# Optimization experiments

Measured on AMD Instinct MI355X. Metric: run time of the kernel, lower is better.

## Reference

```python
import jax, jax.numpy as jnp
import numpy as np

B, T, C, H, N, FFN = 4, 1024, 2048, 32, 64, 7168
HEAD_DIVISOR = 8.0
EPS = 1e-5


def setup_inputs() -> dict:
    key = jax.random.key(0)
    ks = jax.random.split(key, 30)
    rn = lambda k, s, sc=0.02: jax.random.normal(k, s, jnp.float32) * sc
    ru = lambda k, s: jax.random.uniform(k, s, jnp.float32)
    return {
        "x": jax.random.normal(ks[0], (B, T, C), jnp.float32),
        "att_shift": jax.random.normal(ks[1], (B, C), jnp.float32),
        "wkv_state": jax.random.normal(ks[2], (B, H, N, N), jnp.float32) * 0.1,
        "ffn_shift": jax.random.normal(ks[3], (B, C), jnp.float32),
        "ln1_w": jnp.ones((C,), jnp.float32), "ln1_b": jnp.zeros((C,), jnp.float32),
        "ln2_w": jnp.ones((C,), jnp.float32), "ln2_b": jnp.zeros((C,), jnp.float32),
        "mix_k": ru(ks[4], (C,)), "mix_v": ru(ks[5], (C,)),
        "mix_r": ru(ks[6], (C,)), "mix_g": ru(ks[7], (C,)),
        "Wr": rn(ks[8], (C, C)), "Wk": rn(ks[9], (C, C)), "Wv": rn(ks[10], (C, C)),
        "Wg": rn(ks[11], (C, C)), "Wo": rn(ks[12], (C, C)),
        "time_decay": jax.random.normal(ks[13], (H, N), jnp.float32) * 0.5,
        "time_faaaa": jax.random.normal(ks[14], (H, N), jnp.float32) * 0.1,
        "gn_w": jnp.ones((C,), jnp.float32), "gn_b": jnp.zeros((C,), jnp.float32),
        "cmix_k": ru(ks[15], (C,)), "cmix_r": ru(ks[16], (C,)),
        "Wck": rn(ks[17], (C, FFN)), "Wcr": rn(ks[18], (C, C)), "Wcv": rn(ks[19], (FFN, C)),
    }


def _ln(z, w, b):
    m = z.mean(-1, keepdims=True)
    v = z.var(-1, keepdims=True)
    return (z - m) / jnp.sqrt(v + EPS) * w + b


def _shift(x, shift_state):
    # prepend carried last-token state, drop final position
    return jnp.concatenate([shift_state[:, None, :], x[:, :-1]], axis=1)


def reference(x, att_shift, wkv_state, ffn_shift, ln1_w, ln1_b, ln2_w, ln2_b,
              mix_k, mix_v, mix_r, mix_g, Wr, Wk, Wv, Wg, Wo,
              time_decay, time_faaaa, gn_w, gn_b, cmix_k, cmix_r, Wck, Wcr, Wcv):
    Bb, Tt, Cc = x.shape

    # ---- TimeMix ----
    x1 = _ln(x, ln1_w, ln1_b)
    xx = _shift(x1, att_shift)
    xk = x1 * mix_k + xx * (1 - mix_k)
    xv = x1 * mix_v + xx * (1 - mix_v)
    xr = x1 * mix_r + xx * (1 - mix_r)
    xg = x1 * mix_g + xx * (1 - mix_g)
    r = (xr @ Wr).reshape(Bb, Tt, H, N)
    k = (xk @ Wk).reshape(Bb, Tt, H, N)
    v = (xv @ Wv).reshape(Bb, Tt, H, N)
    g = jax.nn.silu(xg @ Wg)

    w = jnp.exp(-jnp.exp(time_decay))[None, :, :, None]  # [1,H,N,1] decay on k-index
    u = time_faaaa[None, :, :, None]                      # [1,H,N,1] bonus on current token

    def step(S, rkv):  # S: [B,H,N,N] (k-index i, v-index j)
        rr, kk, vv = rkv
        kv = kk[..., :, None] * vv[..., None, :]          # [B,H,N,N]
        y = jnp.einsum('bhi,bhij->bhj', rr, S + u * kv)
        return S * w + kv, y

    rkv = (jnp.moveaxis(r, 1, 0), jnp.moveaxis(k, 1, 0), jnp.moveaxis(v, 1, 0))
    new_wkv, ys = jax.lax.scan(step, wkv_state, rkv)      # ys: [T,B,H,N]
    att = jnp.moveaxis(ys, 0, 1)                          # [B,T,H,N]

    # GroupNorm(n_head groups) on att / head_size_divisor
    z = att / HEAD_DIVISOR
    m = z.mean(-1, keepdims=True)
    var = z.var(-1, keepdims=True)
    z = (z - m) / jnp.sqrt(var + EPS)
    z = z * gn_w.reshape(H, N) + gn_b.reshape(H, N)
    att_out = (z.reshape(Bb, Tt, Cc) * g) @ Wo

    x = x + att_out

    # ---- ChannelMix ----
    x2 = _ln(x, ln2_w, ln2_b)
    xx2 = _shift(x2, ffn_shift)
    xck = x2 * cmix_k + xx2 * (1 - cmix_k)
    xcr = x2 * cmix_r + xx2 * (1 - cmix_r)
    kk = jnp.square(jax.nn.relu(xck @ Wck))
    kv = kk @ Wcv
    ffn_out = jax.nn.sigmoid(xcr @ Wcr) * kv
    x = x + ffn_out

    return x, x1[:, -1], new_wkv, x2[:, -1]
```

## Files before the change

kernel.cpp:

```cpp
#include <hip/hip_runtime.h>
#include <cstdint>
#include <cstddef>

typedef unsigned short u16;
typedef unsigned int u32;
typedef short bf16x8 __attribute__((ext_vector_type(8)));
typedef unsigned short u16x4 __attribute__((ext_vector_type(4)));
typedef unsigned short u16x8 __attribute__((ext_vector_type(8)));
typedef float f32x4 __attribute__((ext_vector_type(4)));

#define DEV __device__ __forceinline__

constexpr int Bb = 4, Tt = 1024, Cc = 2048, Hh = 32, Nd = 64, FF = 7168;
constexpr int BT = Bb * Tt;
constexpr int NCH = 16;

DEV u16 f2bf(float f) {
  union { float f; unsigned u; } un; un.f = f;
  unsigned r = un.u + 0x7FFFu + ((un.u >> 16) & 1u);
  return (u16)(r >> 16);
}
DEV float bf2f(u16 h) {
  union { unsigned u; float f; } un; un.u = ((unsigned)h) << 16;
  return un.f;
}
DEV void gll16(const u16* gp, u16* lp) {
  __builtin_amdgcn_global_load_lds(
      (const __attribute__((address_space(1))) unsigned int*)gp,
      (__attribute__((address_space(3))) unsigned int*)lp,
      16, 0, 0);
}

DEV void transp_body(const float* __restrict__ W, u16* __restrict__ Wt,
                     int Kk, int Nn, float (*tile)[33]) {
  int n0 = blockIdx.x * 32, k0 = blockIdx.y * 32;
  int tx = threadIdx.x & 31, ty = threadIdx.x >> 5;
  #pragma unroll
  for (int r = 0; r < 32; r += 8)
    tile[r + ty][tx] = W[(size_t)(k0 + r + ty) * Nn + n0 + tx];
  __syncthreads();
  #pragma unroll
  for (int r = 0; r < 32; r += 8)
    Wt[(size_t)(n0 + r + ty) * Kk + k0 + tx] = f2bf(tile[tx][r + ty]);
}

__global__ void transpose_to_bf16(const float* __restrict__ W, u16* __restrict__ Wt,
                                  int Kk, int Nn) {
  __shared__ float tile[32][33];
  transp_body(W, Wt, Kk, Nn, tile);
}

__global__ void transpose6_cc(const float* __restrict__ W0, const float* __restrict__ W1,
                              const float* __restrict__ W2, const float* __restrict__ W3,
                              const float* __restrict__ W4, const float* __restrict__ W5,
                              u16* __restrict__ T0, u16* __restrict__ T1,
                              u16* __restrict__ T2, u16* __restrict__ T3,
                              u16* __restrict__ T4, u16* __restrict__ T5) {
  __shared__ float tile[32][33];
  const int z = blockIdx.z;
  const float* W = (z == 0) ? W0 : (z == 1) ? W1 : (z == 2) ? W2 :
                   (z == 3) ? W3 : (z == 4) ? W4 : W5;
  u16* T = (z == 0) ? T0 : (z == 1) ? T1 : (z == 2) ? T2 :
           (z == 3) ? T3 : (z == 4) ? T4 : T5;
  transp_body(W, T, Cc, Cc, tile);
}

DEV void block_ln(const float* __restrict__ src, int tid, float* red,
                  float vals[8], float& mean, float& inv) {
  float s = 0.f, ss = 0.f;
  #pragma unroll
  for (int i = 0; i < 8; i++) {
    float t = src[tid + i * 256];
    vals[i] = t; s += t; ss += t * t;
  }
  #pragma unroll
  for (int m = 1; m < 64; m <<= 1) { s += __shfl_xor(s, m); ss += __shfl_xor(ss, m); }
  int lane = tid & 63, wv = tid >> 6;
  __syncthreads();
  if (lane == 0) { red[wv] = s; red[4 + wv] = ss; }
  __syncthreads();
  s = red[0] + red[1] + red[2] + red[3];
  ss = red[4] + red[5] + red[6] + red[7];
  mean = s * (1.f / Cc);
  float var = ss * (1.f / Cc) - mean * mean;
  inv = rsqrtf(var + 1e-5f);
}

__global__ __launch_bounds__(256)
void ln_mix4(const float* __restrict__ x, const float* __restrict__ shift,
             const float* __restrict__ w, const float* __restrict__ b,
             const float* __restrict__ mk, const float* __restrict__ mv,
             const float* __restrict__ mr, const float* __restrict__ mg,
             u16* __restrict__ xk, u16* __restrict__ xv,
             u16* __restrict__ xr, u16* __restrict__ xg,
             float* __restrict__ last) {
  int row = blockIdx.x;
  int t = row & (Tt - 1), bb = row >> 10;
  int tid = threadIdx.x;
  __shared__ float red[8];
  const float* cur = x + (size_t)row * Cc;
  float cv[8], pv[8], cm, ci, pm = 0.f, pi = 1.f;
  block_ln(cur, tid, red, cv, cm, ci);
  bool t0 = (t == 0);
  const float* prev = t0 ? (shift + (size_t)bb * Cc) : (cur - Cc);
  if (!t0) {
    block_ln(prev, tid, red, pv, pm, pi);
  } else {
    #pragma unroll
    for (int i = 0; i < 8; i++) pv[i] = prev[tid + i * 256];
  }
  size_t o = (size_t)row * Cc;
  bool isLast = (t == Tt - 1);
  #pragma unroll
  for (int i = 0; i < 8; i++) {
    int c = tid + i * 256;
    float xc = (cv[i] - cm) * ci * w[c] + b[c];
    float xp = t0 ? pv[i] : (pv[i] - pm) * pi * w[c] + b[c];
    xk[o + c] = f2bf(xp + mk[c] * (xc - xp));
    xv[o + c] = f2bf(xp + mv[c] * (xc - xp));
    xr[o + c] = f2bf(xp + mr[c] * (xc - xp));
    xg[o + c] = f2bf(xp + mg[c] * (xc - xp));
    if (isLast) last[(size_t)bb * Cc + c] = xc;
  }
}

__global__ __launch_bounds__(256)
void ln_mix2(const float* __restrict__ x, const float* __restrict__ shift,
             const float* __restrict__ w, const float* __restrict__ b,
             const float* __restrict__ ck, const float* __restrict__ cr,
             u16* __restrict__ xck, u16* __restrict__ xcr,
             float* __restrict__ last) {
  int row = blockIdx.x;
  int t = row & (Tt - 1), bb = row >> 10;
  int tid = threadIdx.x;
  __shared__ float red[8];
  const float* cur = x + (size_t)row * Cc;
  float cv[8], pv[8], cm, ci, pm = 0.f, pi = 1.f;
  block_ln(cur, tid, red, cv, cm, ci);
  bool t0 = (t == 0);
  const float* prev = t0 ? (shift + (size_t)bb * Cc) : (cur - Cc);
  if (!t0) {
    block_ln(prev, tid, red, pv, pm, pi);
  } else {
    #pragma unroll
    for (int i = 0; i < 8; i++) pv[i] = prev[tid + i * 256];
  }
  size_t o = (size_t)row * Cc;
  bool isLast = (t == Tt - 1);
  #pragma unroll
  for (int i = 0; i < 8; i++) {
    int c = tid + i * 256;
    float xc = (cv[i] - cm) * ci * w[c] + b[c];
    float xp = t0 ? pv[i] : (pv[i] - pm) * pi * w[c] + b[c];
    xck[o + c] = f2bf(xp + ck[c] * (xc - xp));
    xcr[o + c] = f2bf(xp + cr[c] * (xc - xp));
    if (isLast) last[(size_t)bb * Cc + c] = xc;
  }
}


DEV int swzoff(int row, int off) {
  return (row << 7) +
         (off ^ ((((row >> 1) & 1) << 4) | (((row >> 2) & 1) << 5) | (((row >> 3) & 1) << 6)));
}

DEV void stage_half(const u16* __restrict__ gbase, int ldK, u16* slot, int tid) {
  #pragma unroll
  for (int c2 = 0; c2 < 2; c2++) {
    const int D = c2 * 8192 + tid * 16;
    const int row = D >> 7;
    const int off = (D & 127) ^ ((((row >> 1) & 1) << 4) | (((row >> 2) & 1) << 5) | (((row >> 3) & 1) << 6));
    gll16(gbase + (size_t)row * ldK + (off >> 1), (u16*)((char*)slot + D));
  }
}

template <int EPI, int NB>
DEV void g256_core(const u16* __restrict__ A, const u16* __restrict__ Bt,
                   int N, int K,
                   float* __restrict__ Co, u16* __restrict__ Cb,
                   const float* __restrict__ X1, const float* __restrict__ X2,
                   u16 (*lds)[8192], int m0, int n0, int act) {
  const int tid = threadIdx.x;
  const int w = tid >> 6, lane = tid & 63;
  const int l15 = lane & 15, l4 = lane >> 4;
  const int wm = (w & 3) * 64;
  const int wn = (w >> 2) * (NB * 64);
  const int ahalf = wm >> 7;
  const int arow0 = wm & 127;
  const int bhalf = (NB == 2) ? (w >> 2) : 0;
  const int nt = K >> 6;

  const u16* Ag = A + (size_t)m0 * K;
  const u16* Bg = Bt + (size_t)n0 * K;

  f32x4 acc[4][NB * 4] = {};
  bf16x8 a[4][2];

  stage_half(Ag, K, lds[0], tid);
  stage_half(Ag + (size_t)128 * K, K, lds[1], tid);
  stage_half(Bg, K, lds[4], tid);
  if constexpr (NB == 2) stage_half(Bg + (size_t)128 * K, K, lds[5], tid);
  if (nt > 1) {
    stage_half(Ag + 64, K, lds[2], tid);
    stage_half(Ag + (size_t)128 * K + 64, K, lds[3], tid);
    asm volatile("s_waitcnt vmcnt(4)" ::: "memory");
  } else {
    asm volatile("s_waitcnt vmcnt(0)" ::: "memory");
  }
  asm volatile("s_barrier" ::: "memory");

  for (int t = 0; t < nt; t++) {
    const int buf = t & 1;
    const char* Aslot = (const char*)lds[buf * 2 + ahalf];
    const char* Bslot = (const char*)lds[4 + buf * NB + bhalf];

#define G256_PHASE(p)                                                                       \
    {                                                                                       \
      constexpr int nh = (p) >> 1, kh = (p) & 1;                                            \
      if constexpr ((p) < 2) {                                                              \
        _Pragma("unroll")                                                                   \
        for (int mf = 0; mf < 4; mf++) {                                                    \
          const int row = arow0 + mf * 16 + l15;                                            \
          a[mf][kh] = *(const bf16x8*)(Aslot + swzoff(row, kh * 64 + l4 * 16));             \
        }                                                                                   \
      }                                                                                     \
      bf16x8 bfr[2 * NB];                                                                   \
      _Pragma("unroll")                                                                     \
      for (int j = 0; j < 2 * NB; j++) {                                                    \
        const int row = (NB == 2 ? 0 : wn) + (nh * 2 * NB + j) * 16 + l15;                  \
        bfr[j] = *(const bf16x8*)(Bslot + swzoff(row, kh * 64 + l4 * 16));                  \
      }                                                                                     \
      if constexpr ((p) == 0) {                                                             \
        if (t + 1 < nt) stage_half(Bg + (size_t)(t + 1) * 64, K,                            \
                                   lds[4 + ((t + 1) & 1) * NB], tid);                       \
      } else if constexpr ((p) == 1) {                                                      \
        if constexpr (NB == 2) {                                                            \
          if (t + 1 < nt) stage_half(Bg + (size_t)128 * K + (size_t)(t + 1) * 64, K,        \
                                     lds[4 + ((t + 1) & 1) * NB + 1], tid);                 \
        }                                                                                   \
      } else if constexpr ((p) == 2) {                                                      \
        if (t + 2 < nt) stage_half(Ag + (size_t)(t + 2) * 64, K, lds[buf << 1], tid);       \
      } else {                                                                              \
        if (t + 2 < nt) stage_half(Ag + (size_t)128 * K + (size_t)(t + 2) * 64, K,          \
                                   lds[(buf << 1) + 1], tid);                               \
      }                                                                                     \
      asm volatile("s_barrier" ::: "memory");                                               \
      __builtin_amdgcn_s_setprio(1);                                                       \
      _Pragma("unroll")                                                                     \
      for (int mf = 0; mf < 4; mf++)                                                        \
        _Pragma("unroll")                                                                   \
        for (int j = 0; j < 2 * NB; j++)                                                    \
          acc[mf][nh * 2 * NB + j] = __builtin_amdgcn_mfma_f32_16x16x32_bf16(               \
              a[mf][kh], bfr[j], acc[mf][nh * 2 * NB + j], 0, 0, 0);                        \
      __builtin_amdgcn_s_setprio(0);                                                       \
      if constexpr ((p) == 3) {                                                             \
        if (t + 2 < nt) asm volatile("s_waitcnt vmcnt(4)" ::: "memory");                    \
        else            asm volatile("s_waitcnt vmcnt(0)" ::: "memory");                    \
      }                                                                                     \
      asm volatile("s_barrier" ::: "memory");                                               \
    }

    G256_PHASE(0)
    G256_PHASE(1)
    G256_PHASE(2)
    G256_PHASE(3)
#undef G256_PHASE
  }

  #pragma unroll
  for (int mf = 0; mf < 4; mf++) {
    #pragma unroll
    for (int reg = 0; reg < 4; reg++) {
      const int gr = m0 + wm + mf * 16 + l4 * 4 + reg;
      const size_t ro = (size_t)gr * N;
      #pragma unroll
      for (int nf = 0; nf < NB * 4; nf++) {
        const int gc = n0 + wn + nf * 16 + l15;
        float val = acc[mf][nf][reg];
        if constexpr (EPI == 0) {
          Co[ro + gc] = val;
        } else if constexpr (EPI == 1) {
          if (act) val = val / (1.f + __expf(-val));
          Cb[ro + gc] = f2bf(val);
        } else if constexpr (EPI == 3) {
          float tr = fmaxf(val, 0.f);
          Cb[ro + gc] = f2bf(tr * tr);
        } else if constexpr (EPI == 4) {
          Co[ro + gc] = X1[ro + gc] + val;
        } else {
          float s = 1.f / (1.f + __expf(-val));
          Co[ro + gc] = fmaf(s, X2[ro + gc], X1[ro + gc]);
        }
      }
    }
  }
}

template <int EPI>
__global__ __launch_bounds__(512, 2)
void gemm256(const u16* __restrict__ A, const u16* __restrict__ Bt,
             int N, int K,
             float* __restrict__ Co, u16* __restrict__ Cb,
             const float* __restrict__ X1, const float* __restrict__ X2) {
  __shared__ __align__(16) u16 lds[8][8192];
  g256_core<EPI, 2>(A, Bt, N, K, Co, Cb, X1, X2, lds, blockIdx.y * 256, blockIdx.x * 256, 0);
}

template <int EPI>
__global__ __launch_bounds__(512, 2)
void gemm128n(const u16* __restrict__ A, const u16* __restrict__ Bt,
              int N, int K,
              float* __restrict__ Co, u16* __restrict__ Cb,
              const float* __restrict__ X1, const float* __restrict__ X2) {
  __shared__ __align__(16) u16 lds[6][8192];
  g256_core<EPI, 1>(A, Bt, N, K, Co, Cb, X1, X2, lds, blockIdx.y * 256, blockIdx.x * 128, 0);
}

__global__ __launch_bounds__(512, 2)
void gemm256_proj(const u16* __restrict__ A0, const u16* __restrict__ A1,
                  const u16* __restrict__ A2, const u16* __restrict__ A3,
                  const u16* __restrict__ B0, const u16* __restrict__ B1,
                  const u16* __restrict__ B2, const u16* __restrict__ B3,
                  u16* __restrict__ C0, u16* __restrict__ C1,
                  u16* __restrict__ C2, u16* __restrict__ C3) {
  __shared__ __align__(16) u16 lds[8][8192];
  const int z = blockIdx.z;
  const u16* A = (z == 0) ? A0 : (z == 1) ? A1 : (z == 2) ? A2 : A3;
  const u16* Bt = (z == 0) ? B0 : (z == 1) ? B1 : (z == 2) ? B2 : B3;
  u16* Cb = (z == 0) ? C0 : (z == 1) ? C1 : (z == 2) ? C2 : C3;
  g256_core<1, 2>(A, Bt, Cc, Cc, nullptr, Cb, nullptr, nullptr, lds,
                  blockIdx.y * 256, blockIdx.x * 256, z == 3);
}

__global__ __launch_bounds__(256)
void wkv_pre(const u16* __restrict__ rg, const u16* __restrict__ kg,
             const u16* __restrict__ vg, const float* __restrict__ td,
             const float* __restrict__ tf,
             float* __restrict__ Yb, float* __restrict__ Db,
             u16* __restrict__ Rtb) {
  __shared__ float Pt[64][68];
  __shared__ float uL[64];
  __shared__ u16 rB[64 * 72];
  __shared__ u16 kB[64 * 72];
  __shared__ u16 Rh[64 * 72];
  __shared__ u16 KhX[96 * 72];
  __shared__ u16 vA[64 * 72];
  __shared__ u16 Vt[64 * 72];

  const int tid = threadIdx.x, bid = blockIdx.x;
  const int bh = bid >> 4, c = bid & 15;
  const int b = bh >> 5, h = bh & 31;
  const int lane = tid & 63, w = tid >> 6;

  {
    int i = tid & 63;
    float d = __expf(td[h * 64 + i]);
    float c1 = -1.4426950408889634f * d;
    int e0 = (tid >> 6) * 16;
    #pragma unroll
    for (int e = 0; e < 16; e++) Pt[e0 + e][i] = exp2f(c1 * (float)(e0 + e));
    if (tid < 64) uL[tid] = tf[h * 64 + tid];
  }
  __syncthreads();

  const int row = tid >> 2, col0 = (tid & 3) * 16;
  const int tl = row & 15;
  {
    size_t gro = ((size_t)b * Tt + c * 64 + row) * Cc + h * 64 + col0;
    u16x8 rv0 = *(const u16x8*)(rg + gro);
    u16x8 rv1 = *(const u16x8*)(rg + gro + 8);
    u16x8 kv0 = *(const u16x8*)(kg + gro);
    u16x8 kv1 = *(const u16x8*)(kg + gro + 8);
    u16x8 vv0 = *(const u16x8*)(vg + gro);
    u16x8 vv1 = *(const u16x8*)(vg + gro + 8);
    *(u16x8*)&rB[row * 72 + col0] = rv0; *(u16x8*)&rB[row * 72 + col0 + 8] = rv1;
    *(u16x8*)&kB[row * 72 + col0] = kv0; *(u16x8*)&kB[row * 72 + col0 + 8] = kv1;
    *(u16x8*)&vA[row * 72 + col0] = vv0; *(u16x8*)&vA[row * 72 + col0 + 8] = vv1;
    float rf[16], kf[16];
    #pragma unroll
    for (int e = 0; e < 8; e++) { rf[e] = bf2f(rv0[e]); rf[8 + e] = bf2f(rv1[e]); }
    #pragma unroll
    for (int e = 0; e < 8; e++) { kf[e] = bf2f(kv0[e]); kf[8 + e] = bf2f(kv1[e]); }
    u16x8 o0, o1, t0_, t1_;
    #pragma unroll
    for (int e = 0; e < 8; e++) {
      o0[e] = f2bf(rf[e] * Pt[tl][col0 + e]);
      o1[e] = f2bf(rf[8 + e] * Pt[tl][col0 + 8 + e]);
      t0_[e] = f2bf(rf[e] * Pt[row][col0 + e]);
      t1_[e] = f2bf(rf[8 + e] * Pt[row][col0 + 8 + e]);
    }
    *(u16x8*)&Rh[row * 72 + col0] = o0; *(u16x8*)&Rh[row * 72 + col0 + 8] = o1;
    u16* rtp = Rtb + (size_t)bid * 4096 + row * 64 + col0;
    *(u16x8*)rtp = t0_; *(u16x8*)(rtp + 8) = t1_;
    if (row < 48) {
      u16x8 a0, a1;
      #pragma unroll
      for (int e = 0; e < 8; e++) {
        a0[e] = f2bf(kf[e] * Pt[15 - tl][col0 + e]);
        a1[e] = f2bf(kf[8 + e] * Pt[15 - tl][col0 + 8 + e]);
      }
      *(u16x8*)&KhX[row * 72 + col0] = a0; *(u16x8*)&KhX[row * 72 + col0 + 8] = a1;
    }
    if (row < 32) {
      u16x8 a0, a1;
      #pragma unroll
      for (int e = 0; e < 8; e++) {
        a0[e] = f2bf(kf[e] * Pt[31 - tl][col0 + e]);
        a1[e] = f2bf(kf[8 + e] * Pt[31 - tl][col0 + 8 + e]);
      }
      *(u16x8*)&KhX[(48 + row) * 72 + col0] = a0; *(u16x8*)&KhX[(48 + row) * 72 + col0 + 8] = a1;
    }
    if (row < 16) {
      u16x8 a0, a1;
      #pragma unroll
      for (int e = 0; e < 8; e++) {
        a0[e] = f2bf(kf[e] * Pt[47 - tl][col0 + e]);
        a1[e] = f2bf(kf[8 + e] * Pt[47 - tl][col0 + 8 + e]);
      }
      *(u16x8*)&KhX[(80 + row) * 72 + col0] = a0; *(u16x8*)&KhX[(80 + row) * 72 + col0 + 8] = a1;
    }
  }
  __syncthreads();

  {
    const int jj = tid & 63, s0 = (tid >> 6) * 16;
    #pragma unroll
    for (int ds = 0; ds < 16; ds += 2) {
      u32 pk = ((u32)vA[(s0 + ds + 1) * 72 + jj] << 16) | vA[(s0 + ds) * 72 + jj];
      *(u32*)&Vt[jj * 72 + s0 + ds] = pk;
    }
  }
  __syncthreads();

  u16* aB = vA;
  {
    const int pr[6] = {1, 2, 3, 2, 3, 3};
    const int qr[6] = {0, 1, 2, 0, 1, 0};
    const int dr[6] = {0, 0, 0, 1, 1, 2};
    const int lr = lane & 15, kq = lane >> 4;
    for (int pi = w; pi < 6; pi += 4) {
      const int p = pr[pi], q = qr[pi], d = dr[pi];
      const int kbase = (d == 0) ? q * 16 : (d == 1) ? 48 + q * 16 : 80 + q * 16;
      f32x4 aacc = {};
      #pragma unroll
      for (int kf2 = 0; kf2 < 2; kf2++) {
        bf16x8 af = *(const bf16x8*)&Rh[(p * 16 + lr) * 72 + kf2 * 32 + kq * 8];
        bf16x8 bf_ = *(const bf16x8*)&KhX[(kbase + lr) * 72 + kf2 * 32 + kq * 8];
        aacc = __builtin_amdgcn_mfma_f32_16x16x32_bf16(af, bf_, aacc, 0, 0, 0);
      }
      #pragma unroll
      for (int reg = 0; reg < 4; reg++) {
        aB[(p * 16 + kq * 4 + reg) * 72 + q * 16 + lr] = f2bf(aacc[reg]);
        aB[(q * 16 + kq * 4 + reg) * 72 + p * 16 + lr] = 0;
      }
    }
    for (int e = lane; e < 256; e += 64) {
      const int tl2 = e >> 4, sl = e & 15;
      float a = 0.f;
      if (sl <= tl2) {
        const u16* rp = &rB[(w * 16 + tl2) * 72];
        const u16* kp = &kB[(w * 16 + sl) * 72];
        const float* pp = (sl == tl2) ? uL : &Pt[tl2 - 1 - sl][0];
        #pragma unroll
        for (int i0 = 0; i0 < 64; i0 += 4) {
          u16x4 ra = *(const u16x4*)(rp + i0);
          u16x4 ka = *(const u16x4*)(kp + i0);
          f32x4 pa = *(const f32x4*)(pp + i0);
          #pragma unroll
          for (int di = 0; di < 4; di++)
            a = fmaf(bf2f(ra[di]) * bf2f(ka[di]), pa[di], a);
        }
      }
      aB[(w * 16 + tl2) * 72 + w * 16 + sl] = f2bf(a);
    }
  }
  __syncthreads();

  u16* Ktt = KhX;
  {
    const int ii = tid & 63, s0 = (tid >> 6) * 16;
    #pragma unroll
    for (int ds = 0; ds < 16; ds += 2) {
      float v0 = bf2f(kB[(s0 + ds) * 72 + ii]) * Pt[63 - (s0 + ds)][ii];
      float v1 = bf2f(kB[(s0 + ds + 1) * 72 + ii]) * Pt[63 - (s0 + ds + 1)][ii];
      u32 pk = ((u32)f2bf(v1) << 16) | f2bf(v0);
      *(u32*)&Ktt[ii * 72 + s0 + ds] = pk;
    }
  }
  __syncthreads();

  const int lr = lane & 15, kq = lane >> 4;
  {
    f32x4 yac[4] = {};
    #pragma unroll
    for (int kf2 = 0; kf2 < 2; kf2++) {
      bf16x8 af = *(const bf16x8*)&aB[(w * 16 + lr) * 72 + kf2 * 32 + kq * 8];
      #pragma unroll
      for (int nf = 0; nf < 4; nf++) {
        bf16x8 bf_ = *(const bf16x8*)&Vt[(nf * 16 + lr) * 72 + kf2 * 32 + kq * 8];
        yac[nf] = __builtin_amdgcn_mfma_f32_16x16x32_bf16(af, bf_, yac[nf], 0, 0, 0);
      }
    }
    float* Yp = Yb + (size_t)bid * 4096;
    #pragma unroll
    for (int nf = 0; nf < 4; nf++)
      #pragma unroll
      for (int reg = 0; reg < 4; reg++)
        Yp[(w * 16 + kq * 4 + reg) * 64 + nf * 16 + lr] = yac[nf][reg];

    f32x4 dac[4] = {};
    #pragma unroll
    for (int kf2 = 0; kf2 < 2; kf2++) {
      bf16x8 af = *(const bf16x8*)&Ktt[(w * 16 + lr) * 72 + kf2 * 32 + kq * 8];
      #pragma unroll
      for (int nf = 0; nf < 4; nf++) {
        bf16x8 bf_ = *(const bf16x8*)&Vt[(nf * 16 + lr) * 72 + kf2 * 32 + kq * 8];
        dac[nf] = __builtin_amdgcn_mfma_f32_16x16x32_bf16(af, bf_, dac[nf], 0, 0, 0);
      }
    }
    float* Dp = Db + (size_t)bid * 4096;
    #pragma unroll
    for (int nf = 0; nf < 4; nf++)
      #pragma unroll
      for (int reg = 0; reg < 4; reg++)
        Dp[(w * 16 + kq * 4 + reg) * 64 + nf * 16 + lr] = dac[nf][reg];
  }
}

__global__ __launch_bounds__(256)
void wkv_scan(const float* __restrict__ s0g, const float* __restrict__ td,
              const float* __restrict__ Db, u16* __restrict__ Sbb,
              float* __restrict__ sout) {
  const int bh = blockIdx.x, h = bh & 31;
  const int tid = threadIdx.x;
  const int i = tid >> 2, j0 = (tid & 3) * 16;
  float d = __expf(td[h * 64 + i]);
  float w64 = exp2f(-1.4426950408889634f * d * 64.f);
  f32x4 S[4];
  const float* sp = s0g + ((size_t)bh * 64 + i) * 64 + j0;
  #pragma unroll
  for (int q = 0; q < 4; q++) S[q] = *(const f32x4*)(sp + q * 4);
  for (int c = 0; c < NCH; c++) {
    u16* op = Sbb + ((size_t)(bh * 16 + c)) * 4096 + i * 64 + j0;
    u16x8 o0, o1;
    #pragma unroll
    for (int e = 0; e < 4; e++) { o0[e] = f2bf(S[0][e]); o0[4 + e] = f2bf(S[1][e]);
                                  o1[e] = f2bf(S[2][e]); o1[4 + e] = f2bf(S[3][e]); }
    *(u16x8*)op = o0; *(u16x8*)(op + 8) = o1;
    const float* dp = Db + ((size_t)(bh * 16 + c)) * 4096 + i * 64 + j0;
    #pragma unroll
    for (int q = 0; q < 4; q++) {
      f32x4 dv = *(const f32x4*)(dp + q * 4);
      #pragma unroll
      for (int e = 0; e < 4; e++) S[q][e] = fmaf(w64, S[q][e], dv[e]);
    }
  }
  float* fo = sout + ((size_t)bh * 64 + i) * 64 + j0;
  #pragma unroll
  for (int q = 0; q < 4; q++) *(f32x4*)(fo + q * 4) = S[q];
}

__global__ __launch_bounds__(256)
void wkv_post(const u16* __restrict__ Rtb, const u16* __restrict__ Sbb,
              const float* __restrict__ Yb, const u16* __restrict__ g,
              const float* __restrict__ gnw, const float* __restrict__ gnb,
              u16* __restrict__ xo) {
  __shared__ u16 Rt[64 * 72];
  __shared__ u16 St[64 * 72];
  __shared__ u16 xoL[64 * 72];
  const int tid = threadIdx.x, bid = blockIdx.x;
  const int bh = bid >> 4, c = bid & 15;
  const int b = bh >> 5, h = bh & 31;
  const int lane = tid & 63, w = tid >> 6;
  const int row = tid >> 2, col0 = (tid & 3) * 16;

  {
    const u16* rp = Rtb + (size_t)bid * 4096 + row * 64 + col0;
    u16x8 a0 = *(const u16x8*)rp, a1 = *(const u16x8*)(rp + 8);
    *(u16x8*)&Rt[row * 72 + col0] = a0; *(u16x8*)&Rt[row * 72 + col0 + 8] = a1;
  }
  {
    const u16* sp = Sbb + ((size_t)(bh * 16 + c)) * 4096 + row * 64 + col0;
    u16x8 s0 = *(const u16x8*)sp, s1 = *(const u16x8*)(sp + 8);
    #pragma unroll
    for (int e = 0; e < 8; e++) {
      St[(col0 + e) * 72 + row] = s0[e];
      St[(col0 + 8 + e) * 72 + row] = s1[e];
    }
  }
  const int lr = lane & 15, kq = lane >> 4;
  f32x4 acc[4];
  {
    const float* Yp = Yb + (size_t)bid * 4096;
    #pragma unroll
    for (int nf = 0; nf < 4; nf++)
      #pragma unroll
      for (int reg = 0; reg < 4; reg++)
        acc[nf][reg] = Yp[(w * 16 + kq * 4 + reg) * 64 + nf * 16 + lr];
  }
  __syncthreads();
  #pragma unroll
  for (int kf2 = 0; kf2 < 2; kf2++) {
    bf16x8 af = *(const bf16x8*)&Rt[(w * 16 + lr) * 72 + kf2 * 32 + kq * 8];
    #pragma unroll
    for (int nf = 0; nf < 4; nf++) {
      bf16x8 bf_ = *(const bf16x8*)&St[(nf * 16 + lr) * 72 + kf2 * 32 + kq * 8];
      acc[nf] = __builtin_amdgcn_mfma_f32_16x16x32_bf16(af, bf_, acc[nf], 0, 0, 0);
    }
  }
  #pragma unroll
  for (int reg = 0; reg < 4; reg++) {
    float s = 0.f, ss = 0.f;
    #pragma unroll
    for (int nf = 0; nf < 4; nf++) {
      float z = acc[nf][reg] * 0.125f;
      s += z; ss += z * z;
    }
    #pragma unroll
    for (int m = 1; m < 16; m <<= 1) { s += __shfl_xor(s, m); ss += __shfl_xor(ss, m); }
    float mean = s * (1.f / 64.f);
    float var = ss * (1.f / 64.f) - mean * mean;
    float inv = rsqrtf(var + 1e-5f);
    const int tau = w * 16 + kq * 4 + reg;
    #pragma unroll
    for (int nf = 0; nf < 4; nf++) {
      const int col = nf * 16 + lr;
      float z = acc[nf][reg] * 0.125f;
      float zn = (z - mean) * inv * gnw[h * 64 + col] + gnb[h * 64 + col];
      float gv = bf2f(g[((size_t)b * Tt + c * 64 + tau) * Cc + h * 64 + col]);
      xoL[tau * 72 + col] = f2bf(zn * gv);
    }
  }
  __syncthreads();
  {
    u16x8 o0 = *(const u16x8*)&xoL[row * 72 + col0];
    u16x8 o1 = *(const u16x8*)&xoL[row * 72 + col0 + 8];
    u16* xop = xo + ((size_t)b * Tt + c * 64 + row) * Cc + h * 64 + col0;
    *(u16x8*)xop = o0; *(u16x8*)(xop + 8) = o1;
  }
}

extern "C" void kernel_launch(void* const* d_in, const int* in_sizes, int n_in,
                              void* d_out, int out_size, void* d_ws, size_t ws_size,
                              hipStream_t stream) {
  const float* x         = (const float*)d_in[0];
  const float* att_shift = (const float*)d_in[1];
  const float* wkv0      = (const float*)d_in[2];
  const float* ffn_shift = (const float*)d_in[3];
  const float* ln1w = (const float*)d_in[4];
  const float* ln1b = (const float*)d_in[5];
  const float* ln2w = (const float*)d_in[6];
  const float* ln2b = (const float*)d_in[7];
  const float* mixk = (const float*)d_in[8];
  const float* mixv = (const float*)d_in[9];
  const float* mixr = (const float*)d_in[10];
  const float* mixg = (const float*)d_in[11];
  const float* Wr = (const float*)d_in[12];
  const float* Wk = (const float*)d_in[13];
  const float* Wv = (const float*)d_in[14];
  const float* Wg = (const float*)d_in[15];
  const float* Wo = (const float*)d_in[16];
  const float* td = (const float*)d_in[17];
  const float* tf = (const float*)d_in[18];
  const float* gnw = (const float*)d_in[19];
  const float* gnb = (const float*)d_in[20];
  const float* cmk = (const float*)d_in[21];
  const float* cmr = (const float*)d_in[22];
  const float* Wck = (const float*)d_in[23];
  const float* Wcr = (const float*)d_in[24];
  const float* Wcv = (const float*)d_in[25];

  constexpr size_t SZ_CC = (size_t)Cc * Cc * 2;
  constexpr size_t SZ_CF = (size_t)Cc * FF * 2;
  constexpr size_t SZ_AB = (size_t)BT * Cc * 2;
  constexpr size_t O_W   = 0;
  constexpr size_t O_R1  = 6 * SZ_CC + 2 * SZ_CF;
  constexpr size_t R1_SZ = 4 * SZ_AB;
  constexpr size_t O_R2  = O_R1 + R1_SZ;
  constexpr size_t R2_SZ = 3 * SZ_AB;
  constexpr size_t O_R3  = O_R2 + R2_SZ;
  constexpr size_t WS_NEED = O_R3 + SZ_AB;

  if (ws_size < WS_NEED) return;

  char* ws = (char*)d_ws;
  u16* WrT  = (u16*)(ws + O_W);
  u16* WkT  = (u16*)(ws + O_W + 1 * SZ_CC);
  u16* WvT  = (u16*)(ws + O_W + 2 * SZ_CC);
  u16* WgT  = (u16*)(ws + O_W + 3 * SZ_CC);
  u16* WoT  = (u16*)(ws + O_W + 4 * SZ_CC);
  u16* WcrT = (u16*)(ws + O_W + 5 * SZ_CC);
  u16* WckT = (u16*)(ws + O_W + 6 * SZ_CC);
  u16* WcvT = (u16*)(ws + O_W + 6 * SZ_CC + SZ_CF);

  u16*   xk  = (u16*)(ws + O_R1);
  u16*   xv  = (u16*)(ws + O_R1 + SZ_AB);
  u16*   xr  = (u16*)(ws + O_R1 + 2 * SZ_AB);
  u16*   xg  = (u16*)(ws + O_R1 + 3 * SZ_AB);
  float* Yb  = (float*)(ws + O_R1);
  u16*   Rtb = (u16*)(ws + O_R1 + 2 * SZ_AB);
  u16*   Sbb = (u16*)(ws + O_R1 + 3 * SZ_AB);
  u16*   kk  = (u16*)(ws + O_R1);
  u16*   rb  = (u16*)(ws + O_R2);
  u16*   kb  = (u16*)(ws + O_R2 + SZ_AB);
  u16*   vb  = (u16*)(ws + O_R2 + 2 * SZ_AB);
  u16*   xo  = (u16*)(ws + O_R2);
  u16*   xck = (u16*)(ws + O_R2 + SZ_AB);
  u16*   xcr = (u16*)(ws + O_R2 + 2 * SZ_AB);
  float* kv  = (float*)(ws + O_R2);
  u16*   gbuf = (u16*)(ws + O_R3);

  float* out      = (float*)d_out;
  float* x1_last  = out + (size_t)BT * Cc;
  float* wkv_out  = x1_last + (size_t)Bb * Cc;
  float* x2_last  = wkv_out + (size_t)Bb * Hh * Nd * Nd;
  float* Db       = out;

  transpose6_cc<<<dim3(64, 64, 6), 256, 0, stream>>>(Wr, Wk, Wv, Wg, Wo, Wcr,
                                                     WrT, WkT, WvT, WgT, WoT, WcrT);
  transpose_to_bf16<<<dim3(224, 64), 256, 0, stream>>>(Wck, WckT, Cc, FF);
  transpose_to_bf16<<<dim3(64, 224), 256, 0, stream>>>(Wcv, WcvT, FF, Cc);

  ln_mix4<<<BT, 256, 0, stream>>>(x, att_shift, ln1w, ln1b,
                                  mixk, mixv, mixr, mixg, xk, xv, xr, xg, x1_last);
  gemm256_proj<<<dim3(8, 16, 4), 512, 0, stream>>>(xr, xk, xv, xg,
                                                   WrT, WkT, WvT, WgT,
                                                   rb, kb, vb, gbuf);
  wkv_pre<<<Bb * Hh * NCH, 256, 0, stream>>>(rb, kb, vb, td, tf, Yb, Db, Rtb);
  wkv_scan<<<Bb * Hh, 256, 0, stream>>>(wkv0, td, Db, Sbb, wkv_out);
  wkv_post<<<Bb * Hh * NCH, 256, 0, stream>>>(Rtb, Sbb, Yb, gbuf, gnw, gnb, xo);
  gemm128n<4><<<dim3(16, 16), 512, 0, stream>>>(xo, WoT, Cc, Cc, out, nullptr, x, nullptr);
  ln_mix2<<<BT, 256, 0, stream>>>(out, ffn_shift, ln2w, ln2b, cmk, cmr, xck, xcr, x2_last);
  gemm256<3><<<dim3(28, 16), 512, 0, stream>>>(xck, WckT, FF, Cc, nullptr, kk, nullptr, nullptr);
  gemm128n<0><<<dim3(16, 16), 512, 0, stream>>>(kk, WcvT, Cc, FF, kv, nullptr, nullptr, nullptr);
  gemm128n<5><<<dim3(16, 16), 512, 0, stream>>>(xcr, WcrT, Cc, Cc, out, nullptr, out, kv);

  (void)in_sizes; (void)n_in; (void)out_size;
}
```

Before: 735.3 us.

## Split-K the FFN value GEMM and XCD-swizzle block order for all GEMMs

```diff
diff --git a/kernel.cpp b/kernel.cpp
--- a/kernel.cpp
+++ b/kernel.cpp
@@ -29,6 +29,10 @@
       (const __attribute__((address_space(1))) unsigned int*)gp,
       (__attribute__((address_space(3))) unsigned int*)lp,
       16, 0, 0);
+}
+DEV int xcd_swz(int f, int nwg) {
+  int q = nwg >> 3;
+  return (f & 7) * q + (f >> 3);
 }
 
 DEV void transp_body(const float* __restrict__ W, u16* __restrict__ Wt,
@@ -158,7 +162,6 @@
   }
 }
 
-
 DEV int swzoff(int row, int off) {
   return (row << 7) +
          (off ^ ((((row >> 1) & 1) << 4) | (((row >> 2) & 1) << 5) | (((row >> 3) & 1) << 6)));
@@ -176,9 +179,10 @@
 
 template <int EPI, int NB>
 DEV void g256_core(const u16* __restrict__ A, const u16* __restrict__ Bt,
-                   int N, int K,
+                   int N, int K, int ldK,
                    float* __restrict__ Co, u16* __restrict__ Cb,
                    const float* __restrict__ X1, const float* __restrict__ X2,
+                   const u16* __restrict__ X2b,
                    u16 (*lds)[8192], int m0, int n0, int act) {
   const int tid = threadIdx.x;
   const int w = tid >> 6, lane = tid & 63;
@@ -190,19 +194,19 @@
   const int bhalf = (NB == 2) ? (w >> 2) : 0;
   const int nt = K >> 6;
 
-  const u16* Ag = A + (size_t)m0 * K;
-  const u16* Bg = Bt + (size_t)n0 * K;
+  const u16* Ag = A + (size_t)m0 * ldK;
+  const u16* Bg = Bt + (size_t)n0 * ldK;
 
   f32x4 acc[4][NB * 4] = {};
   bf16x8 a[4][2];
 
-  stage_half(Ag, K, lds[0], tid);
-  stage_half(Ag + (size_t)128 * K, K, lds[1], tid);
-  stage_half(Bg, K, lds[4], tid);
-  if constexpr (NB == 2) stage_half(Bg + (size_t)128 * K, K, lds[5], tid);
+  stage_half(Ag, ldK, lds[0], tid);
+  stage_half(Ag + (size_t)128 * ldK, ldK, lds[1], tid);
+  stage_half(Bg, ldK, lds[4], tid);
+  if constexpr (NB == 2) stage_half(Bg + (size_t)128 * ldK, ldK, lds[5], tid);
   if (nt > 1) {
-    stage_half(Ag + 64, K, lds[2], tid);
-    stage_half(Ag + (size_t)128 * K + 64, K, lds[3], tid);
+    stage_half(Ag + 64, ldK, lds[2], tid);
+    stage_half(Ag + (size_t)128 * ldK + 64, ldK, lds[3], tid);
     asm volatile("s_waitcnt vmcnt(4)" ::: "memory");
   } else {
     asm volatile("s_waitcnt vmcnt(0)" ::: "memory");
@@ -231,17 +235,17 @@
         bfr[j] = *(const bf16x8*)(Bslot + swzoff(row, kh * 64 + l4 * 16));                  \
       }                                                                                     \
       if constexpr ((p) == 0) {                                                             \
-        if (t + 1 < nt) stage_half(Bg + (size_t)(t + 1) * 64, K,                            \
+        if (t + 1 < nt) stage_half(Bg + (size_t)(t + 1) * 64, ldK,                          \
                                    lds[4 + ((t + 1) & 1) * NB], tid);                       \
       } else if constexpr ((p) == 1) {                                                      \
         if constexpr (NB == 2) {                                                            \
-          if (t + 1 < nt) stage_half(Bg + (size_t)128 * K + (size_t)(t + 1) * 64, K,        \
+          if (t + 1 < nt) stage_half(Bg + (size_t)128 * ldK + (size_t)(t + 1) * 64, ldK,    \
                                      lds[4 + ((t + 1) & 1) * NB + 1], tid);                 \
         }                                                                                   \
       } else if constexpr ((p) == 2) {                                                      \
-        if (t + 2 < nt) stage_half(Ag + (size_t)(t + 2) * 64, K, lds[buf << 1], tid);       \
+        if (t + 2 < nt) stage_half(Ag + (size_t)(t + 2) * 64, ldK, lds[buf << 1], tid);     \
       } else {                                                                              \
-        if (t + 2 < nt) stage_half(Ag + (size_t)128 * K + (size_t)(t + 2) * 64, K,          \
+        if (t + 2 < nt) stage_half(Ag + (size_t)128 * ldK + (size_t)(t + 2) * 64, ldK,      \
                                    lds[(buf << 1) + 1], tid);                               \
       }                                                                                     \
       asm volatile("s_barrier" ::: "memory");                                               \
@@ -289,7 +293,8 @@
           Co[ro + gc] = X1[ro + gc] + val;
         } else {
           float s = 1.f / (1.f + __expf(-val));
-          Co[ro + gc] = fmaf(s, X2[ro + gc], X1[ro + gc]);
+          float kvv = X2[ro + gc] + bf2f(X2b[ro + gc]);
+          Co[ro + gc] = fmaf(s, kvv, X1[ro + gc]);
         }
       }
     }
@@ -297,26 +302,33 @@
 }
 
 template <int EPI>
-__global__ __launch_bounds__(512, 2)
-void gemm256(const u16* __restrict__ A, const u16* __restrict__ Bt,
-             int N, int K,
-             float* __restrict__ Co, u16* __restrict__ Cb,
-             const float* __restrict__ X1, const float* __restrict__ X2) {
-  __shared__ __align__(16) u16 lds[8][8192];
-  g256_core<EPI, 2>(A, Bt, N, K, Co, Cb, X1, X2, lds, blockIdx.y * 256, blockIdx.x * 256, 0);
-}
-
-template <int EPI>
-__global__ __launch_bounds__(512, 2)
-void gemm128n(const u16* __restrict__ A, const u16* __restrict__ Bt,
+__global__ __launch_bounds__(512)
+void gemm256s(const u16* __restrict__ A, const u16* __restrict__ Bt,
               int N, int K,
               float* __restrict__ Co, u16* __restrict__ Cb,
-              const float* __restrict__ X1, const float* __restrict__ X2) {
+              const float* __restrict__ X1, int NX) {
+  __shared__ __align__(16) u16 lds[8][8192];
+  int o = xcd_swz(blockIdx.x, gridDim.x);
+  int xb = o % NX, yb = o / NX;
+  g256_core<EPI, 2>(A, Bt, N, K, K, Co, Cb, X1, nullptr, nullptr, lds,
+                    yb * 256, xb * 256, 0);
+}
+
+template <int EPI>
+__global__ __launch_bounds__(512)
+void gemm128s(const u16* __restrict__ A, const u16* __restrict__ Bt,
+              int N, int K,
+              float* __restrict__ Co, u16* __restrict__ Cb,
+              const float* __restrict__ X1, const float* __restrict__ X2,
+              const u16* __restrict__ X2b, int NX) {
   __shared__ __align__(16) u16 lds[6][8192];
-  g256_core<EPI, 1>(A, Bt, N, K, Co, Cb, X1, X2, lds, blockIdx.y * 256, blockIdx.x * 128, 0);
-}
-
-__global__ __launch_bounds__(512, 2)
+  int o = xcd_swz(blockIdx.x, gridDim.x);
+  int xb = o % NX, yb = o / NX;
+  g256_core<EPI, 1>(A, Bt, N, K, K, Co, Cb, X1, X2, X2b, lds,
+                    yb * 256, xb * 128, 0);
+}
+
+__global__ __launch_bounds__(512)
 void gemm256_proj(const u16* __restrict__ A0, const u16* __restrict__ A1,
                   const u16* __restrict__ A2, const u16* __restrict__ A3,
                   const u16* __restrict__ B0, const u16* __restrict__ B1,
@@ -324,12 +336,28 @@
                   u16* __restrict__ C0, u16* __restrict__ C1,
                   u16* __restrict__ C2, u16* __restrict__ C3) {
   __shared__ __align__(16) u16 lds[8][8192];
-  const int z = blockIdx.z;
+  int o = xcd_swz(blockIdx.x, gridDim.x);
+  int xb = o & 7, yb = (o >> 3) & 15, z = o >> 7;
   const u16* A = (z == 0) ? A0 : (z == 1) ? A1 : (z == 2) ? A2 : A3;
   const u16* Bt = (z == 0) ? B0 : (z == 1) ? B1 : (z == 2) ? B2 : B3;
   u16* Cb = (z == 0) ? C0 : (z == 1) ? C1 : (z == 2) ? C2 : C3;
-  g256_core<1, 2>(A, Bt, Cc, Cc, nullptr, Cb, nullptr, nullptr, lds,
-                  blockIdx.y * 256, blockIdx.x * 256, z == 3);
+  g256_core<1, 2>(A, Bt, Cc, Cc, Cc, nullptr, Cb, nullptr, nullptr, nullptr, lds,
+                  yb * 256, xb * 256, z == 3);
+}
+
+__global__ __launch_bounds__(512)
+void gemm256_splitk(const u16* __restrict__ A, const u16* __restrict__ Bt,
+                    float* __restrict__ kv0, u16* __restrict__ kv1) {
+  __shared__ __align__(16) u16 lds[8][8192];
+  int o = xcd_swz(blockIdx.x, gridDim.x);
+  int xb = o & 7, yb = (o >> 3) & 15, z = o >> 7;
+  const int Koff = z * (FF / 2);
+  if (z == 0)
+    g256_core<0, 2>(A + Koff, Bt + Koff, Cc, FF / 2, FF, kv0, nullptr,
+                    nullptr, nullptr, nullptr, lds, yb * 256, xb * 256, 0);
+  else
+    g256_core<1, 2>(A + Koff, Bt + Koff, Cc, FF / 2, FF, nullptr, kv1,
+                    nullptr, nullptr, nullptr, lds, yb * 256, xb * 256, 0);
 }
 
 __global__ __launch_bounds__(256)
@@ -704,11 +732,12 @@
   u16*   rb  = (u16*)(ws + O_R2);
   u16*   kb  = (u16*)(ws + O_R2 + SZ_AB);
   u16*   vb  = (u16*)(ws + O_R2 + 2 * SZ_AB);
-  u16*   xo  = (u16*)(ws + O_R2);
+  u16*   xcr = (u16*)(ws + O_R2);
   u16*   xck = (u16*)(ws + O_R2 + SZ_AB);
-  u16*   xcr = (u16*)(ws + O_R2 + 2 * SZ_AB);
-  float* kv  = (float*)(ws + O_R2);
+  u16*   xo  = (u16*)(ws + O_R2 + 2 * SZ_AB);
+  float* kv0 = (float*)(ws + O_R2 + SZ_AB);
   u16*   gbuf = (u16*)(ws + O_R3);
+  u16*   kv1  = (u16*)(ws + O_R3);
 
   float* out      = (float*)d_out;
   float* x1_last  = out + (size_t)BT * Cc;
@@ -723,17 +752,19 @@
 
   ln_mix4<<<BT, 256, 0, stream>>>(x, att_shift, ln1w, ln1b,
                                   mixk, mixv, mixr, mixg, xk, xv, xr, xg, x1_last);
-  gemm256_proj<<<dim3(8, 16, 4), 512, 0, stream>>>(xr, xk, xv, xg,
-                                                   WrT, WkT, WvT, WgT,
-                                                   rb, kb, vb, gbuf);
+  gemm256_proj<<<512, 512, 0, stream>>>(xr, xk, xv, xg,
+                                        WrT, WkT, WvT, WgT,
+                                        rb, kb, vb, gbuf);
   wkv_pre<<<Bb * Hh * NCH, 256, 0, stream>>>(rb, kb, vb, td, tf, Yb, Db, Rtb);
   wkv_scan<<<Bb * Hh, 256, 0, stream>>>(wkv0, td, Db, Sbb, wkv_out);
   wkv_post<<<Bb * Hh * NCH, 256, 0, stream>>>(Rtb, Sbb, Yb, gbuf, gnw, gnb, xo);
-  gemm128n<4><<<dim3(16, 16), 512, 0, stream>>>(xo, WoT, Cc, Cc, out, nullptr, x, nullptr);
+  gemm128s<4><<<256, 512, 0, stream>>>(xo, WoT, Cc, Cc, out, nullptr, x,
+                                       nullptr, nullptr, 16);
   ln_mix2<<<BT, 256, 0, stream>>>(out, ffn_shift, ln2w, ln2b, cmk, cmr, xck, xcr, x2_last);
-  gemm256<3><<<dim3(28, 16), 512, 0, stream>>>(xck, WckT, FF, Cc, nullptr, kk, nullptr, nullptr);
-  gemm128n<0><<<dim3(16, 16), 512, 0, stream>>>(kk, WcvT, Cc, FF, kv, nullptr, nullptr, nullptr);
-  gemm128n<5><<<dim3(16, 16), 512, 0, stream>>>(xcr, WcrT, Cc, Cc, out, nullptr, out, kv);
+  gemm256s<3><<<448, 512, 0, stream>>>(xck, WckT, FF, Cc, nullptr, kk, nullptr, 28);
+  gemm256_splitk<<<256, 512, 0, stream>>>(kk, WcvT, kv0, kv1);
+  gemm128s<6><<<256, 512, 0, stream>>>(xcr, WcrT, Cc, Cc, out, nullptr, out,
+                                       kv0, kv1, 16);
 
   (void)in_sizes; (void)n_in; (void)out_size;
 }
```

Result: no change. 724.5 us (-1.5%).
